# Performance work log

Measured on AMD Instinct MI355X. Metric: run time of the kernel, lower is better.

Reference implementation:

```python
import jax, jax.numpy as jnp
import numpy as np
from jax import lax


def setup_inputs() -> dict:
    key = jax.random.key(0)
    ks = jax.random.split(key, 5)
    B, N, F = 16, 2048, 64
    S, P, O = 4, 22, 42  # n_dimensions, n_propagate, n_filters
    x = jax.random.normal(ks[0], (B, N, F), dtype=jnp.float32)
    W_s = jax.random.normal(ks[1], (F, S), dtype=jnp.float32) * (1.0 / np.sqrt(F))
    b_s = jnp.zeros((S,), dtype=jnp.float32)
    W_f = jax.random.normal(ks[2], (F, P), dtype=jnp.float32) * (1.0 / np.sqrt(F))
    b_f = jnp.zeros((P,), dtype=jnp.float32)
    W_o = jax.random.normal(ks[3], (F + 2 * P, O), dtype=jnp.float32) * (1.0 / np.sqrt(F + 2 * P))
    b_o = jnp.zeros((O,), dtype=jnp.float32)
    return {"x": x, "W_s": W_s, "b_s": b_s, "W_f": W_f, "b_f": b_f,
            "W_o": W_o, "b_o": b_o, "n_neighbours": 40}


def reference(x, W_s, b_s, W_f, b_f, W_o, b_o, n_neighbours):
    # x: [B, N, F]
    coords = x @ W_s + b_s            # [B, N, S]   spatial transform
    feats = x @ W_f + b_f             # [B, N, P]   feature transform (FLR)
    # pairwise squared distances: [B, N, N]
    d2 = jnp.sum((coords[:, :, None, :] - coords[:, None, :, :]) ** 2, axis=-1)
    # k nearest (top_k of -distance); drop self (slot 0)
    neg_d, idx = lax.top_k(-d2, n_neighbours)        # [B, N, k]
    dist = -neg_d[:, :, 1:]                          # [B, N, k-1]
    nbr_idx = idx[:, :, 1:]                          # [B, N, k-1]
    weights = jnp.exp(-dist)[..., None]              # [B, N, k-1, 1]
    # batched gather of neighbour features: [B, N, k-1, P]
    nbr_feats = jax.vmap(lambda f, i: f[i])(feats, nbr_idx)
    weighted = nbr_feats * weights
    n_max = jnp.max(weighted, axis=2)                # [B, N, P]
    n_mean = jnp.mean(weighted, axis=2)              # [B, N, P]
    updated = jnp.concatenate([x, n_max, n_mean], axis=-1)  # [B, N, F+2P]
    return jnp.tanh(updated @ W_o + b_o)             # [B, N, n_filters]
```

## Files before the change

### kernel.cpp

```cpp
#include <hip/hip_runtime.h>
#include <math.h>

#define BB 16
#define NN 2048
#define FF 64
#define SS 4
#define PP 22
#define OO 42
#define FPDIM (FF + 2*PP)
#define NREG 32

__device__ __forceinline__ float readfirstlane_f32(float v) {
    return __uint_as_float((unsigned)__builtin_amdgcn_readfirstlane((int)__float_as_uint(v)));
}

__device__ __forceinline__ int wave_scan_dpp(int x) {
    x += __builtin_amdgcn_update_dpp(0, x, 0x111, 0xf, 0xf, true);
    x += __builtin_amdgcn_update_dpp(0, x, 0x112, 0xf, 0xf, true);
    x += __builtin_amdgcn_update_dpp(0, x, 0x114, 0xf, 0xf, true);
    x += __builtin_amdgcn_update_dpp(0, x, 0x118, 0xf, 0xf, true);
    x += __builtin_amdgcn_update_dpp(0, x, 0x142, 0xa, 0xf, true);
    x += __builtin_amdgcn_update_dpp(0, x, 0x143, 0xc, 0xf, true);
    return x;
}
__device__ __forceinline__ int wave_sum_dpp(int x) {
    return __builtin_amdgcn_readlane(wave_scan_dpp(x), 63);
}
__device__ __forceinline__ float wave_fsum_dpp(float x) {
    float t;
    t = __uint_as_float((unsigned)__builtin_amdgcn_update_dpp(0, (int)__float_as_uint(x), 0x111, 0xf, 0xf, true)); x += t;
    t = __uint_as_float((unsigned)__builtin_amdgcn_update_dpp(0, (int)__float_as_uint(x), 0x112, 0xf, 0xf, true)); x += t;
    t = __uint_as_float((unsigned)__builtin_amdgcn_update_dpp(0, (int)__float_as_uint(x), 0x114, 0xf, 0xf, true)); x += t;
    t = __uint_as_float((unsigned)__builtin_amdgcn_update_dpp(0, (int)__float_as_uint(x), 0x118, 0xf, 0xf, true)); x += t;
    t = __uint_as_float((unsigned)__builtin_amdgcn_update_dpp(0, (int)__float_as_uint(x), 0x142, 0xa, 0xf, true)); x += t;
    t = __uint_as_float((unsigned)__builtin_amdgcn_update_dpp(0, (int)__float_as_uint(x), 0x143, 0xc, 0xf, true)); x += t;
    return __uint_as_float((unsigned)__builtin_amdgcn_readlane((int)__float_as_uint(x), 63));
}

__global__ __launch_bounds__(256) void precompute_kernel(
    const float* __restrict__ x, const float* __restrict__ Ws, const float* __restrict__ bs,
    const float* __restrict__ Wf, const float* __restrict__ bf,
    float* __restrict__ coords, float* __restrict__ feats)
{
    int row = blockIdx.x * 256 + threadIdx.x;
    if (row >= BB * NN) return;

    const float4* x4 = (const float4*)(x + (size_t)row * FF);
    float c0 = bs[0], c1 = bs[1], c2 = bs[2], c3 = bs[3];
    float f[PP];
    #pragma unroll
    for (int c = 0; c < PP; c++) f[c] = bf[c];

    #pragma unroll
    for (int k4 = 0; k4 < FF / 4; k4++) {
        float4 xv = x4[k4];
        float xs[4] = {xv.x, xv.y, xv.z, xv.w};
        #pragma unroll
        for (int r = 0; r < 4; r++) {
            int k = k4 * 4 + r;
            float xk = xs[r];
            c0 = fmaf(xk, Ws[k * SS + 0], c0);
            c1 = fmaf(xk, Ws[k * SS + 1], c1);
            c2 = fmaf(xk, Ws[k * SS + 2], c2);
            c3 = fmaf(xk, Ws[k * SS + 3], c3);
            #pragma unroll
            for (int c = 0; c < PP; c++) f[c] = fmaf(xk, Wf[k * PP + c], f[c]);
        }
    }
    float4* cp = (float4*)(coords + (size_t)row * SS);
    *cp = make_float4(c0, c1, c2, c3);
    float* fo = feats + (size_t)row * PP;
    #pragma unroll
    for (int c = 0; c < PP; c++) fo[c] = f[c];
}

__global__ __launch_bounds__(128, 4) void knn_out_kernel(
    const float* __restrict__ coords, const float* __restrict__ feats,
    const float* __restrict__ x, const float* __restrict__ Wo, const float* __restrict__ bo,
    const int* __restrict__ nnbr, float* __restrict__ out)
{
    const int lane = threadIdx.x & 63;
    const int w    = threadIdx.x >> 6;
    const int q    = blockIdx.x * 2 + w;
    const int b    = q >> 11;
    const int i    = q & (NN - 1);

    int K = *nnbr; K = K < 2 ? 2 : (K > 64 ? 64 : K);

    __shared__ int   isel[2][64];
    __shared__ float wsel[2][64];
    __shared__ unsigned long long candk[2][64];
    __shared__ __align__(16) float urow[2][112];

    const float4* cb = (const float4*)(coords + (size_t)b * NN * SS);
    float4 qv = cb[i];
    const float qx = readfirstlane_f32(qv.x);
    const float qy = readfirstlane_f32(qv.y);
    const float qz = readfirstlane_f32(qv.z);
    const float qw = readfirstlane_f32(qv.w);

    float d2r[NREG];
    float lmin = INFINITY;
    #pragma unroll 4
    for (int r = 0; r < NREG; r++) {
        float4 c = cb[r * 64 + lane];
        float d0 = qx - c.x, d1 = qy - c.y, d2 = qz - c.z, d3 = qw - c.w;
        float v = d0 * d0 + d1 * d1 + d2 * d2 + d3 * d3;
        d2r[r] = v;
        lmin = fminf(lmin, v);
    }
    urow[w][lane] = x[((size_t)b * NN + i) * FF + lane];
    __builtin_amdgcn_wave_barrier();

    float t0 = wave_fsum_dpp(lmin) * (1.0f / 64.0f);

    unsigned loU = 0u, hiU = 0x7F800000u;
    int cLo = 0, cHi = NN;
    int laneLo = 0, laneHi = NREG;
    float tPrev = t0; int cPrev = -1;
    int probes = 0;
    while (cHi - cLo > 64 && hiU - loU > 1u && probes < 20) {
        unsigned tAU = 0u, tBU = 0u;
        bool fell = false;
        if (probes == 0) {
            if (t0 > 0.f) { tAU = __float_as_uint(t0 * 0.80f); tBU = __float_as_uint(t0 * 1.30f); }
            else fell = true;
        } else if (cPrev > 0) {
            float g = tPrev * __fsqrt_rn((float)K / (float)cPrev);
            tAU = __float_as_uint(g * 0.88f); tBU = __float_as_uint(g * 1.18f);
        } else if (cPrev == 0) {
            tAU = __float_as_uint(tPrev * 3.0f); tBU = __float_as_uint(tPrev * 9.0f);
        } else fell = true;
        unsigned span = hiU - loU;
        if (fell || !(tAU > loU && tAU < hiU)) tAU = loU + span / 3u;
        if (tAU <= loU) tAU = loU + 1u;
        if (tAU >= hiU) tAU = hiU - 1u;
        if (fell || !(tBU >= tAU && tBU < hiU)) tBU = tAU + (hiU - tAU) / 2u;
        if (tBU < tAU) tBU = tAU;
        if (tBU >= hiU) tBU = hiU - 1u;

        float tA = __uint_as_float(tAU), tB = __uint_as_float(tBU);
        int clA = 0, clB = 0;
        #pragma unroll
        for (int r = 0; r < NREG; r++) {
            clA += (d2r[r] < tA) ? 1 : 0;
            clB += (d2r[r] < tB) ? 1 : 0;
        }
        int tot = wave_sum_dpp(clA | (clB << 16));
        int cA = tot & 0xFFFF, cB = tot >> 16;

        if (cA >= K) { hiU = tAU; cHi = cA; laneHi = clA; }
        else {
            loU = tAU; cLo = cA; laneLo = clA;
            if (cB >= K) { hiU = tBU; cHi = cB; laneHi = clB; }
            else         { loU = tBU; cLo = cB; laneLo = clB; }
        }
        int dA = cA > K ? cA - K : K - cA;
        int dB = cB > K ? cB - K : K - cB;
        if (cA > 0 && dA <= dB) { tPrev = tA; cPrev = cA; }
        else                    { tPrev = tB; cPrev = cB; }
        probes++;
    }

    const float lo = __uint_as_float(loU);
    const float hi = __uint_as_float(hiU);
    const int  need = K - cLo;

    int c1 = laneLo;
    int c2 = laneHi - laneLo;
    if (lane == (i & 63) && loU > 0u) c1 -= 1;
    int pk = c1 | (c2 << 16);
    int inc = wave_scan_dpp(pk);
    int excl = inc - pk;
    int tot  = __builtin_amdgcn_readlane(inc, 63);
    int b1 = excl & 0xFFFF;
    int b2 = excl >> 16;
    const int nbelow = tot & 0xFFFF;
    int ecand = tot >> 16; if (ecand > 64) ecand = 64;
    #pragma unroll
    for (int r = 0; r < NREG; r++) {
        float v = d2r[r];
        int j = r * 64 + lane;
        if ((v < lo) & (j != i)) { isel[w][b1] = j; wsel[w][b1] = v; b1++; }
        else if ((v >= lo) & (v < hi)) { if (b2 < 64) candk[w][b2] = ((unsigned long long)__float_as_uint(v) << 32) | (unsigned)j; b2++; }
    }
    __builtin_amdgcn_wave_barrier();

    int nsel;
    if (ecand == need && loU > 0u) {
        if (lane < ecand) {
            int slot = nbelow + lane;
            if (slot < 64) {
                unsigned long long k2 = candk[w][lane];
                isel[w][slot] = (int)(k2 & 0xFFFFFFFFull);
                wsel[w][slot] = __uint_as_float((unsigned)(k2 >> 32));
            }
        }
        nsel = nbelow + ecand;
        if (nsel > 64) nsel = 64;
    } else {
        unsigned long long mykey = ~0ull;
        if (lane < ecand) mykey = candk[w][lane];
        int mr = 0;
        for (int u = 0; u < ecand; u++) {
            unsigned long long k2 = candk[w][u];
            mr += (k2 < mykey) ? 1 : 0;
        }
        int mj = (int)(mykey & 0xFFFFFFFFull);
        bool ps = (lane < ecand) & (mr < need) & (mj != i);
        unsigned long long ms = __ballot(ps);
        if (ps) {
            int slot = nbelow + __popcll(ms & ((1ull << lane) - 1ull));
            if (slot < 64) { isel[w][slot] = mj; wsel[w][slot] = __uint_as_float((unsigned)(mykey >> 32)); }
        }
        nsel = nbelow + __popcll(ms);
        if (nsel > 64) nsel = 64;
    }
    __builtin_amdgcn_wave_barrier();
    if (lane < nsel) wsel[w][lane] = __expf(-wsel[w][lane]);
    __builtin_amdgcn_wave_barrier();

    const float* fb = feats + (size_t)b * NN * PP;
    int g = lane >> 5, c = lane & 31;
    float mx = -INFINITY, sm = 0.f;
    if (c < PP) {
        #pragma unroll 4
        for (int m = g; m < nsel; m += 2) {
            int j = isel[w][m]; float wt = wsel[w][m];
            float f = fb[(size_t)j * PP + c];
            float wf = wt * f;
            mx = fmaxf(mx, wf); sm += wf;
        }
    }
    float mx2 = __shfl_xor(mx, 32, 64);
    float sm2 = __shfl_xor(sm, 32, 64);
    mx = fmaxf(mx, mx2); sm += sm2;
    if (g == 0 && c < PP) {
        urow[w][FF + c]      = mx;
        urow[w][FF + PP + c] = sm / (float)(K - 1);
    }
    __builtin_amdgcn_wave_barrier();

    if (lane < OO) {
        float a0 = bo[lane], a1 = 0.f, a2 = 0.f, a3 = 0.f;
        const float* wo = Wo + lane;
        #pragma unroll
        for (int k4 = 0; k4 < FPDIM / 4; k4++) {
            float4 u = *((const float4*)&urow[w][k4 * 4]);
            a0 = fmaf(u.x, wo[(k4 * 4 + 0) * OO], a0);
            a1 = fmaf(u.y, wo[(k4 * 4 + 1) * OO], a1);
            a2 = fmaf(u.z, wo[(k4 * 4 + 2) * OO], a2);
            a3 = fmaf(u.w, wo[(k4 * 4 + 3) * OO], a3);
        }
        float acc = (a0 + a1) + (a2 + a3);
        float a = acc < -12.f ? -12.f : (acc > 12.f ? 12.f : acc);
        float e2 = __expf(2.f * a);
        out[(size_t)q * OO + lane] = (e2 - 1.f) / (e2 + 1.f);
    }
}

extern "C" void kernel_launch(void* const* d_in, const int* in_sizes, int n_in,
                              void* d_out, int out_size, void* d_ws, size_t ws_size,
                              hipStream_t stream) {
    const float* x  = (const float*)d_in[0];
    const float* Ws = (const float*)d_in[1];
    const float* bs = (const float*)d_in[2];
    const float* Wf = (const float*)d_in[3];
    const float* bf = (const float*)d_in[4];
    const float* Wo = (const float*)d_in[5];
    const float* bo = (const float*)d_in[6];
    const int*   nn = (const int*)d_in[7];
    float* out = (float*)d_out;

    float* coords = (float*)d_ws;
    float* feats  = coords + (size_t)BB * NN * SS;

    precompute_kernel<<<(BB * NN) / 256, 256, 0, stream>>>(x, Ws, bs, Wf, bf, coords, feats);
    knn_out_kernel<<<(BB * NN) / 2, 128, 0, stream>>>(coords, feats, x, Wo, bo, nn, out);
}
```

Before: 186.0 us.

## Hoist x·Wo partial product into precompute and use four-threshold initial probe

Splits the output projection so the x-part (x @ Wo[:F] + bo) is computed in the precompute kernel alongside coords and feats and stored in workspace. The kNN kernel then only multiplies the 44 neighbour-aggregate features, and it no longer loads x or stages it in shared memory. The first threshold-search round now counts four thresholds around the mean minimum distance in one register pass, replacing the two-threshold probe, to narrow the bracket with fewer passes. The gather loop unroll is raised. The trade-off is a heavier precompute kernel with 42 extra accumulators per thread, which adds register pressure, plus extra workspace traffic.

```diff
diff --git a/kernel.cpp b/kernel.cpp
--- a/kernel.cpp
+++ b/kernel.cpp
@@ -40,7 +40,8 @@
 __global__ __launch_bounds__(256) void precompute_kernel(
     const float* __restrict__ x, const float* __restrict__ Ws, const float* __restrict__ bs,
     const float* __restrict__ Wf, const float* __restrict__ bf,
-    float* __restrict__ coords, float* __restrict__ feats)
+    const float* __restrict__ Wo, const float* __restrict__ bo,
+    float* __restrict__ coords, float* __restrict__ feats, float* __restrict__ xwo)
 {
     int row = blockIdx.x * 256 + threadIdx.x;
     if (row >= BB * NN) return;
@@ -50,8 +51,11 @@
     float f[PP];
     #pragma unroll
     for (int c = 0; c < PP; c++) f[c] = bf[c];
-
-    #pragma unroll
+    float o42[OO];
+    #pragma unroll
+    for (int o = 0; o < OO; o++) o42[o] = bo[o];
+
+    #pragma unroll 4
     for (int k4 = 0; k4 < FF / 4; k4++) {
         float4 xv = x4[k4];
         float xs[4] = {xv.x, xv.y, xv.z, xv.w};
@@ -65,6 +69,8 @@
             c3 = fmaf(xk, Ws[k * SS + 3], c3);
             #pragma unroll
             for (int c = 0; c < PP; c++) f[c] = fmaf(xk, Wf[k * PP + c], f[c]);
+            #pragma unroll
+            for (int o = 0; o < OO; o++) o42[o] = fmaf(xk, Wo[k * OO + o], o42[o]);
         }
     }
     float4* cp = (float4*)(coords + (size_t)row * SS);
@@ -72,11 +78,14 @@
     float* fo = feats + (size_t)row * PP;
     #pragma unroll
     for (int c = 0; c < PP; c++) fo[c] = f[c];
+    float* xo = xwo + (size_t)row * OO;
+    #pragma unroll
+    for (int o = 0; o < OO; o++) xo[o] = o42[o];
 }
 
 __global__ __launch_bounds__(128, 4) void knn_out_kernel(
     const float* __restrict__ coords, const float* __restrict__ feats,
-    const float* __restrict__ x, const float* __restrict__ Wo, const float* __restrict__ bo,
+    const float* __restrict__ xwo, const float* __restrict__ Wo,
     const int* __restrict__ nnbr, float* __restrict__ out)
 {
     const int lane = threadIdx.x & 63;
@@ -90,7 +99,10 @@
     __shared__ int   isel[2][64];
     __shared__ float wsel[2][64];
     __shared__ unsigned long long candk[2][64];
-    __shared__ __align__(16) float urow[2][112];
+    __shared__ __align__(16) float urow[2][48];
+
+    float xw = 0.f;
+    if (lane < OO) xw = xwo[(size_t)q * OO + lane];
 
     const float4* cb = (const float4*)(coords + (size_t)b * NN * SS);
     float4 qv = cb[i];
@@ -109,8 +121,6 @@
         d2r[r] = v;
         lmin = fminf(lmin, v);
     }
-    urow[w][lane] = x[((size_t)b * NN + i) * FF + lane];
-    __builtin_amdgcn_wave_barrier();
 
     float t0 = wave_fsum_dpp(lmin) * (1.0f / 64.0f);
 
@@ -118,14 +128,45 @@
     int cLo = 0, cHi = NN;
     int laneLo = 0, laneHi = NREG;
     float tPrev = t0; int cPrev = -1;
+
+    if (t0 > 1e-30f) {
+        float t1 = t0 * 0.75f, t2 = t0 * 0.95f, t3 = t0 * 1.15f, t4 = t0 * 1.40f;
+        int l1 = 0, l2 = 0, l3 = 0, l4 = 0;
+        #pragma unroll
+        for (int r = 0; r < NREG; r++) {
+            float v = d2r[r];
+            l1 += (v < t1) ? 1 : 0;
+            l2 += (v < t2) ? 1 : 0;
+            l3 += (v < t3) ? 1 : 0;
+            l4 += (v < t4) ? 1 : 0;
+        }
+        int s12 = wave_sum_dpp(l1 | (l2 << 16));
+        int s34 = wave_sum_dpp(l3 | (l4 << 16));
+        int c1 = s12 & 0xFFFF, c2 = s12 >> 16, c3 = s34 & 0xFFFF, c4 = s34 >> 16;
+        if (c1 >= K)      { hiU = __float_as_uint(t1); cHi = c1; laneHi = l1; }
+        else if (c2 >= K) { loU = __float_as_uint(t1); cLo = c1; laneLo = l1;
+                            hiU = __float_as_uint(t2); cHi = c2; laneHi = l2; }
+        else if (c3 >= K) { loU = __float_as_uint(t2); cLo = c2; laneLo = l2;
+                            hiU = __float_as_uint(t3); cHi = c3; laneHi = l3; }
+        else if (c4 >= K) { loU = __float_as_uint(t3); cLo = c3; laneLo = l3;
+                            hiU = __float_as_uint(t4); cHi = c4; laneHi = l4; }
+        else              { loU = __float_as_uint(t4); cLo = c4; laneLo = l4; }
+        int bc = -1, bd = 0x7FFFFFFF; float bt = t0;
+        int cs[4] = {c1, c2, c3, c4}; float ts[4] = {t1, t2, t3, t4};
+        #pragma unroll
+        for (int u = 0; u < 4; u++) {
+            int d = cs[u] > K ? cs[u] - K : K - cs[u];
+            if (cs[u] > 0 && d < bd) { bd = d; bc = cs[u]; bt = ts[u]; }
+        }
+        if (bc > 0) { tPrev = bt; cPrev = bc; }
+        else        { tPrev = t4; cPrev = 0; }
+    }
+
     int probes = 0;
     while (cHi - cLo > 64 && hiU - loU > 1u && probes < 20) {
         unsigned tAU = 0u, tBU = 0u;
         bool fell = false;
-        if (probes == 0) {
-            if (t0 > 0.f) { tAU = __float_as_uint(t0 * 0.80f); tBU = __float_as_uint(t0 * 1.30f); }
-            else fell = true;
-        } else if (cPrev > 0) {
+        if (cPrev > 0) {
             float g = tPrev * __fsqrt_rn((float)K / (float)cPrev);
             tAU = __float_as_uint(g * 0.88f); tBU = __float_as_uint(g * 1.18f);
         } else if (cPrev == 0) {
@@ -166,10 +207,10 @@
     const float hi = __uint_as_float(hiU);
     const int  need = K - cLo;
 
-    int c1 = laneLo;
-    int c2 = laneHi - laneLo;
-    if (lane == (i & 63) && loU > 0u) c1 -= 1;
-    int pk = c1 | (c2 << 16);
+    int c1c = laneLo;
+    int c2c = laneHi - laneLo;
+    if (lane == (i & 63) && loU > 0u) c1c -= 1;
+    int pk = c1c | (c2c << 16);
     int inc = wave_scan_dpp(pk);
     int excl = inc - pk;
     int tot  = __builtin_amdgcn_readlane(inc, 63);
@@ -224,7 +265,7 @@
     int g = lane >> 5, c = lane & 31;
     float mx = -INFINITY, sm = 0.f;
     if (c < PP) {
-        #pragma unroll 4
+        #pragma unroll 8
         for (int m = g; m < nsel; m += 2) {
             int j = isel[w][m]; float wt = wsel[w][m];
             float f = fb[(size_t)j * PP + c];
@@ -236,16 +277,16 @@
     float sm2 = __shfl_xor(sm, 32, 64);
     mx = fmaxf(mx, mx2); sm += sm2;
     if (g == 0 && c < PP) {
-        urow[w][FF + c]      = mx;
-        urow[w][FF + PP + c] = sm / (float)(K - 1);
+        urow[w][c]      = mx;
+        urow[w][PP + c] = sm / (float)(K - 1);
     }
     __builtin_amdgcn_wave_barrier();
 
     if (lane < OO) {
-        float a0 = bo[lane], a1 = 0.f, a2 = 0.f, a3 = 0.f;
-        const float* wo = Wo + lane;
-        #pragma unroll
-        for (int k4 = 0; k4 < FPDIM / 4; k4++) {
+        float a0 = xw, a1 = 0.f, a2 = 0.f, a3 = 0.f;
+        const float* wo = Wo + FF * OO + lane;
+        #pragma unroll
+        for (int k4 = 0; k4 < (2 * PP) / 4; k4++) {
             float4 u = *((const float4*)&urow[w][k4 * 4]);
             a0 = fmaf(u.x, wo[(k4 * 4 + 0) * OO], a0);
             a1 = fmaf(u.y, wo[(k4 * 4 + 1) * OO], a1);
@@ -274,7 +315,8 @@
 
     float* coords = (float*)d_ws;
     float* feats  = coords + (size_t)BB * NN * SS;
-
-    precompute_kernel<<<(BB * NN) / 256, 256, 0, stream>>>(x, Ws, bs, Wf, bf, coords, feats);
-    knn_out_kernel<<<(BB * NN) / 2, 128, 0, stream>>>(coords, feats, x, Wo, bo, nn, out);
-}
+    float* xwo    = feats  + (size_t)BB * NN * PP;
+
+    precompute_kernel<<<(BB * NN) / 256, 256, 0, stream>>>(x, Ws, bs, Wf, bf, Wo, bo, coords, feats, xwo);
+    knn_out_kernel<<<(BB * NN) / 2, 128, 0, stream>>>(coords, feats, xwo, Wo, nn, out);
+}
```

New measurement: 194.3 us. 4.4% more time.
